# Performance work log

Hardware: AMD Instinct MI355X
Metric: run time of the kernel (lower is better)

Reference implementation:

```python
import jax, jax.numpy as jnp
import numpy as np

B, N, D, V, Y = 4, 2048, 300, 50000, 20000
MAX_REL = 10
LN_EPS = 1e-5


def setup_inputs() -> dict:
    key = jax.random.key(0)
    k1, k2, k3, k4, k5 = jax.random.split(key, 5)
    M_s = jax.random.randint(k1, (B, N), 0, V, dtype=jnp.int64)
    s = 1.0 / np.sqrt(D)
    E_v = jax.random.normal(k2, (V, D), dtype=jnp.float32) * s
    E_v = E_v.at[0].set(0.0)  # padding_idx=0
    E_y = jax.random.normal(k3, (Y, D), dtype=jnp.float32) * s
    E_y = E_y.at[0].set(0.0)
    W_A = jax.random.normal(k4, (D, D), dtype=jnp.float32) * s
    W_O = jax.random.normal(k5, (D, D), dtype=jnp.float32) * s
    gamma = jnp.ones((D,), dtype=jnp.float32)
    beta = jnp.zeros((D,), dtype=jnp.float32)
    return {"M_s": M_s, "E_v": E_v, "E_y": E_y, "W_A": W_A, "W_O": W_O,
            "gamma": gamma, "beta": beta}


def reference(M_s, E_v, E_y, W_A, W_O, gamma, beta):
    # Embedding lookup (dropout is identity in eval / p=0)
    X = E_v[M_s]                                   # [B, N, D]
    Q = X                                          # self-attention mode (v_q=None)
    # weights = Q @ W_A @ X^T
    QW = jnp.einsum('bnd,de->bne', Q, W_A)         # [B, N, D]
    weights = jnp.einsum('bne,bme->bnm', QW, X)    # [B, N, N]
    # relative-distance bias (clipped |i-j|)
    r = jnp.arange(N)
    dist = jnp.clip(jnp.abs(r[None, :] - r[:, None]), 0, MAX_REL).astype(weights.dtype)
    weights = weights - dist
    # padding mask over context (key) positions
    mask = (M_s != 0)                              # [B, N]
    weights = jnp.where(mask[:, None, :], weights, -jnp.inf)
    A = jax.nn.softmax(weights, axis=-1)           # [B, N, N]
    # contextualized query + output projection
    Q_c = jnp.einsum('bnm,bmd->bnd', A, X) @ W_O   # [B, N, D]
    # residual + layernorm over D
    H = Q_c + Q
    mu = jnp.mean(H, axis=-1, keepdims=True)
    var = jnp.mean((H - mu) ** 2, axis=-1, keepdims=True)
    Hn = (H - mu) * jax.lax.rsqrt(var + LN_EPS) * gamma + beta
    # vocab projection over senses
    y_logits = Hn @ E_y.T                          # [B, N, Y]
    return y_logits, A
```

## Files before the change

kernel.cpp:

```cpp
#include <hip/hip_runtime.h>
#include <hip/hip_bf16.h>

#define B_ 4
#define N_ 2048
#define D_ 300
#define Y_ 20000
#define ROWS (B_*N_)

typedef __attribute__((ext_vector_type(8))) short bf16x8;
typedef __attribute__((ext_vector_type(4))) float f32x4;

__device__ __forceinline__ unsigned short f2bf(float f) {
  unsigned u = __float_as_uint(f);
  unsigned r = (u + 0x7FFFu + ((u >> 16) & 1u)) >> 16;
  return (unsigned short)r;
}

__device__ __forceinline__ void gl_lds16(const unsigned short* g, unsigned short* l) {
  __builtin_amdgcn_global_load_lds(
      (const __attribute__((address_space(1))) void*)g,
      (__attribute__((address_space(3))) void*)l, 16, 0, 0);
}

__global__ __launch_bounds__(256) void k_gather_pack(const int* __restrict__ M_s,
    const float* __restrict__ E_v, float* __restrict__ X,
    unsigned short* __restrict__ Xp) {
  __shared__ float xs[320];
  int row = blockIdx.x, tid = threadIdx.x;
  int tok = M_s[row];
  const float* src = E_v + (size_t)tok * D_;
  for (int d = tid; d < 320; d += 256) xs[d] = (d < D_) ? src[d] : 0.f;
  __syncthreads();
  float* dst = X + (size_t)row * D_;
  for (int d = tid; d < D_; d += 256) dst[d] = xs[d];
  if (tid < 40) {
    int kt = tid >> 2, j = tid & 3;
    int tile = row >> 7, fb = (row >> 4) & 7, rl = row & 15;
    unsigned short v[8];
    #pragma unroll
    for (int e = 0; e < 8; ++e) v[e] = f2bf(xs[kt*32 + j*8 + e]);
    size_t off_ = ((size_t)(tile*10 + kt))*4096 + fb*512 + rl*8 + j*128;
    ushort4* o = (ushort4*)&Xp[off_];
    o[0] = make_ushort4(v[0],v[1],v[2],v[3]);
    o[1] = make_ushort4(v[4],v[5],v[6],v[7]);
  }
}

__global__ __launch_bounds__(256) void k_pack(const float* __restrict__ src,
    unsigned short* __restrict__ dst, int nrows, int ncols, int KT) {
  int chunk = blockIdx.x;
  int tile = chunk / KT, kt = chunk - tile*KT;
  size_t obase = (size_t)chunk * 4096;
  #pragma unroll
  for (int p = 0; p < 2; ++p) {
    int idx = p*256 + threadIdx.x;
    int fb = idx >> 6, l = idx & 63;
    int row = tile*128 + fb*16 + (l & 15);
    int gk = kt*32 + (l >> 4)*8;
    unsigned short v[8];
    #pragma unroll
    for (int e = 0; e < 8; ++e) {
      int k = gk + e;
      float f = (row < nrows && k < ncols) ? src[(size_t)row*ncols + k] : 0.f;
      v[e] = f2bf(f);
    }
    ushort4* o = (ushort4*)&dst[obase + (size_t)idx*8];
    o[0] = make_ushort4(v[0],v[1],v[2],v[3]);
    o[1] = make_ushort4(v[4],v[5],v[6],v[7]);
  }
}

__global__ __launch_bounds__(256) void k_packT(const float* __restrict__ src,
    unsigned short* __restrict__ dst, int src_rows, int src_cols, int KT,
    size_t src_bstride, size_t dst_bchunks) {
  __shared__ float ls[32*133];
  int chunk = blockIdx.x, b = blockIdx.y, tid = threadIdx.x;
  const float* s = src + (size_t)b * src_bstride;
  unsigned short* d = dst + ((size_t)b * dst_bchunks + chunk) * 4096;
  int tile = chunk / KT, kt = chunk - tile*KT;
  int c0 = tile*128, k0 = kt*32;
  for (int i = tid; i < 4096; i += 256) {
    int r = i >> 7, c = i & 127;
    int sr = k0 + r, sc = c0 + c;
    ls[r*133 + c] = (sr < src_rows && sc < src_cols) ? s[(size_t)sr*src_cols + sc] : 0.f;
  }
  __syncthreads();
  #pragma unroll
  for (int p = 0; p < 2; ++p) {
    int idx = p*256 + tid;
    int fb = idx >> 6, l = idx & 63;
    int r = fb*16 + (l & 15);
    int kl = (l >> 4)*8;
    unsigned short v[8];
    #pragma unroll
    for (int e = 0; e < 8; ++e) v[e] = f2bf(ls[(kl + e)*133 + r]);
    ushort4* o = (ushort4*)&d[(size_t)idx*8];
    o[0] = make_ushort4(v[0],v[1],v[2],v[3]);
    o[1] = make_ushort4(v[4],v[5],v[6],v[7]);
  }
}

template<int EPI, bool NT>
__global__ __launch_bounds__(256) void k_gemm(
    const unsigned short* __restrict__ Ap, const unsigned short* __restrict__ Bp,
    float* __restrict__ out, const float* __restrict__ resid,
    const int* __restrict__ Ms, int KT, int MTB, int NTB, int ncols)
{
  __shared__ __align__(16) union {
    unsigned short stage[2][2][4096];
    float epi[64*132];
  } sm;
  const int nt = blockIdx.x, mt = blockIdx.y, z = blockIdx.z;
  const int tid = threadIdx.x;
  const int wave = tid >> 6, lane = tid & 63;
  const int wm = wave >> 1, wn = wave & 1;
  const unsigned short* Ab = Ap + (size_t)(z*MTB + mt) * KT * 4096;
  const unsigned short* Bb = Bp + (size_t)(z*NTB + nt) * KT * 4096;
  f32x4 acc[4][4] = {};

  auto stage = [&](int s, int kt) {
    const unsigned short* ga = Ab + kt*4096 + wave*1024 + lane*8;
    const unsigned short* gb = Bb + kt*4096 + wave*1024 + lane*8;
    unsigned short* la = &sm.stage[s][0][wave*1024];
    unsigned short* lb = &sm.stage[s][1][wave*1024];
    gl_lds16(ga,       la);
    gl_lds16(ga + 512, la + 512);
    gl_lds16(gb,       lb);
    gl_lds16(gb + 512, lb + 512);
  };

  stage(0, 0);
  __syncthreads();
  for (int kt = 0; kt < KT; ++kt) {
    int cur = kt & 1;
    if (kt + 1 < KT) stage(cur ^ 1, kt + 1);
    bf16x8 af[4], bfr[4];
    #pragma unroll
    for (int i = 0; i < 4; ++i)
      af[i] = *(const bf16x8*)&sm.stage[cur][0][(wm*4 + i)*512 + lane*8];
    #pragma unroll
    for (int i = 0; i < 4; ++i)
      bfr[i] = *(const bf16x8*)&sm.stage[cur][1][(wn*4 + i)*512 + lane*8];
    #pragma unroll
    for (int mi = 0; mi < 4; ++mi)
      #pragma unroll
      for (int ni = 0; ni < 4; ++ni)
        acc[mi][ni] = __builtin_amdgcn_mfma_f32_16x16x32_bf16(
            af[mi], bfr[ni], acc[mi][ni], 0, 0, 0);
    __syncthreads();
  }

  const int lr0 = (lane >> 4) << 2;
  const int lc0 = wn*64 + (lane & 15);
  const size_t growbase = ((size_t)(z*MTB + mt)) << 7;
  #pragma unroll
  for (int h = 0; h < 2; ++h) {
    if (wm == h) {
      int tok[4];
      if (EPI == 1) {
        #pragma unroll
        for (int ni = 0; ni < 4; ++ni)
          tok[ni] = Ms[z*N_ + (nt<<7) + lc0 + ni*16];
      }
      #pragma unroll
      for (int mi = 0; mi < 4; ++mi) {
        #pragma unroll
        for (int ni = 0; ni < 4; ++ni) {
          int col = lc0 + ni*16;
          #pragma unroll
          for (int r = 0; r < 4; ++r) {
            int row = lr0 + mi*16 + r;
            float v = acc[mi][ni][r];
            if (EPI == 1) {
              int rb = (mt<<7) + h*64 + row;
              int gc = (nt<<7) + col;
              int dd = rb - gc; if (dd < 0) dd = -dd; if (dd > 10) dd = 10;
              v -= (float)dd;
              if (tok[ni] == 0) v = -3.0e38f;
            }
            sm.epi[row*132 + col] = v;
          }
        }
      }
    }
    __syncthreads();
    {
      const int r0 = tid >> 5;
      const int c4 = (tid & 31) << 2;
      const int gc = (nt << 7) + c4;
      #pragma unroll
      for (int rr = r0; rr < 64; rr += 8) {
        size_t grow = growbase + h*64 + rr;
        if (gc + 3 < ncols) {
          f32x4 v = *(const f32x4*)&sm.epi[rr*132 + c4];
          if (EPI == 2) v += *(const f32x4*)&resid[grow*(size_t)ncols + gc];
          if (NT) __builtin_nontemporal_store(v, (f32x4*)&out[grow*(size_t)ncols + gc]);
          else    *(f32x4*)&out[grow*(size_t)ncols + gc] = v;
        } else {
          #pragma unroll
          for (int e = 0; e < 4; ++e) {
            int c = gc + e;
            if (c < ncols) {
              float v = sm.epi[rr*132 + c4 + e];
              if (EPI == 2) v += resid[grow*(size_t)ncols + c];
              if (NT) __builtin_nontemporal_store(v, &out[grow*(size_t)ncols + c]);
              else    out[grow*(size_t)ncols + c] = v;
            }
          }
        }
      }
    }
    __syncthreads();
  }
}

__global__ __launch_bounds__(256) void k_softmax(float* __restrict__ S,
    unsigned short* __restrict__ Apk) {
  __shared__ float w[N_];
  __shared__ float red[4];
  int row = blockIdx.x, tid = threadIdx.x;
  float* sr = S + (size_t)row * N_;
  float vmax = -3.4e38f;
  for (int m = tid; m < N_; m += 256) { float v = sr[m]; w[m] = v; vmax = fmaxf(vmax, v); }
  #pragma unroll
  for (int off = 32; off; off >>= 1) vmax = fmaxf(vmax, __shfl_down(vmax, off, 64));
  if ((tid & 63) == 0) red[tid >> 6] = vmax;
  __syncthreads();
  vmax = fmaxf(fmaxf(red[0], red[1]), fmaxf(red[2], red[3]));
  float vsum = 0.f;
  for (int m = tid; m < N_; m += 256) {
    float e = __expf(w[m] - vmax);
    w[m] = e;
    vsum += e;
  }
  #pragma unroll
  for (int off = 32; off; off >>= 1) vsum += __shfl_down(vsum, off, 64);
  __syncthreads();
  if ((tid & 63) == 0) red[tid >> 6] = vsum;
  __syncthreads();
  float inv = 1.f / ((red[0] + red[1]) + (red[2] + red[3]));
  for (int m = tid; m < N_; m += 256)
    __builtin_nontemporal_store(w[m] * inv, &sr[m]);
  int kt = tid >> 2, j = tid & 3;
  int m0 = kt*32 + j*8;
  int fb = (row >> 4) & 7, rl = row & 15;
  unsigned short v[8];
  #pragma unroll
  for (int e = 0; e < 8; ++e) v[e] = f2bf(w[m0 + e] * inv);
  size_t off_ = ((size_t)((row >> 7)*64 + kt))*4096 + fb*512 + rl*8 + j*128;
  ushort4* o = (ushort4*)&Apk[off_];
  o[0] = make_ushort4(v[0],v[1],v[2],v[3]);
  o[1] = make_ushort4(v[4],v[5],v[6],v[7]);
}

__global__ __launch_bounds__(320) void k_ln_pack(const float* __restrict__ H,
    const float* __restrict__ gamma, const float* __restrict__ beta,
    unsigned short* __restrict__ Hp) {
  __shared__ float red[5];
  __shared__ float hs[320];
  int row = blockIdx.x, tid = threadIdx.x;
  float h = (tid < D_) ? H[(size_t)row*D_ + tid] : 0.f;
  float s = h;
  #pragma unroll
  for (int off = 32; off; off >>= 1) s += __shfl_down(s, off, 64);
  if ((tid & 63) == 0) red[tid >> 6] = s;
  __syncthreads();
  float mu = (red[0]+red[1]+red[2]+red[3]+red[4]) * (1.f/(float)D_);
  float dv = (tid < D_) ? (h - mu) : 0.f;
  float s2 = dv * dv;
  #pragma unroll
  for (int off = 32; off; off >>= 1) s2 += __shfl_down(s2, off, 64);
  __syncthreads();
  if ((tid & 63) == 0) red[tid >> 6] = s2;
  __syncthreads();
  float var = (red[0]+red[1]+red[2]+red[3]+red[4]) * (1.f/(float)D_);
  float rstd = rsqrtf(var + 1e-5f);
  hs[tid] = (tid < D_) ? (dv * rstd * gamma[tid] + beta[tid]) : 0.f;
  __syncthreads();
  if (tid < 40) {
    int kt = tid >> 2, j = tid & 3;
    int tile = row >> 7, fb = (row >> 4) & 7, rl = row & 15;
    unsigned short v[8];
    #pragma unroll
    for (int e = 0; e < 8; ++e) v[e] = f2bf(hs[kt*32 + j*8 + e]);
    size_t off_ = ((size_t)(tile*10 + kt))*4096 + fb*512 + rl*8 + j*128;
    ushort4* o = (ushort4*)&Hp[off_];
    o[0] = make_ushort4(v[0],v[1],v[2],v[3]);
    o[1] = make_ushort4(v[4],v[5],v[6],v[7]);
  }
}

extern "C" void kernel_launch(void* const* d_in, const int* in_sizes, int n_in,
                              void* d_out, int out_size, void* d_ws, size_t ws_size,
                              hipStream_t stream) {
  const int*   M_s   = (const int*)d_in[0];
  const float* E_v   = (const float*)d_in[1];
  const float* E_y   = (const float*)d_in[2];
  const float* W_A   = (const float*)d_in[3];
  const float* W_O   = (const float*)d_in[4];
  const float* gamma = (const float*)d_in[5];
  const float* beta  = (const float*)d_in[6];

  float* Yl = (float*)d_out;
  float* A  = Yl + (size_t)ROWS * Y_;

  float* X  = (float*)d_ws;
  float* QW = X  + (size_t)ROWS * D_;
  float* C  = QW;
  float* H  = QW + (size_t)ROWS * D_;
  unsigned short* Ep = (unsigned short*)(H + (size_t)ROWS * D_);
  unsigned short* Hpk = (unsigned short*)X;

  unsigned short* scr = (unsigned short*)(Yl + 100000000ull);
  unsigned short* Xp  = scr;
  unsigned short* QWp = Xp  + 2621440;
  unsigned short* Wap = QWp + 2621440;
  unsigned short* Wop = Wap + 122880;
  unsigned short* XTp = Wop + 122880;
  unsigned short* Cp  = XTp + 3145728;
  unsigned short* Apk = Cp  + 2621440;

  k_gather_pack<<<ROWS, 256, 0, stream>>>(M_s, E_v, X, Xp);
  k_packT <<<dim3(3*10,1), 256, 0, stream>>>(W_A, Wap, D_, D_, 10, 0, 0);
  k_gemm<0,false><<<dim3(3,64,1), 256, 0, stream>>>(Xp, Wap, QW, nullptr, nullptr, 10, 64, 3, D_);
  k_pack  <<<64*10, 256, 0, stream>>>(QW, QWp, ROWS, D_, 10);
  k_gemm<1,false><<<dim3(16,16,4), 256, 0, stream>>>(QWp, Xp, A, nullptr, M_s, 10, 16, 16, N_);
  k_softmax<<<ROWS, 256, 0, stream>>>(A, Apk);
  k_packT <<<dim3(3*64,4), 256, 0, stream>>>(X, XTp, N_, D_, 64, (size_t)N_*D_, 192);
  k_gemm<0,false><<<dim3(3,16,4), 256, 0, stream>>>(Apk, XTp, C, nullptr, nullptr, 64, 16, 3, D_);
  k_pack  <<<64*10, 256, 0, stream>>>(C, Cp, ROWS, D_, 10);
  k_packT <<<dim3(3*10,1), 256, 0, stream>>>(W_O, Wop, D_, D_, 10, 0, 0);
  k_gemm<2,false><<<dim3(3,64,1), 256, 0, stream>>>(Cp, Wop, H, X, nullptr, 10, 64, 3, D_);
  k_ln_pack<<<ROWS, 320, 0, stream>>>(H, gamma, beta, Hpk);
  k_pack  <<<157*10, 256, 0, stream>>>(E_y, Ep, Y_, D_, 10);
  k_gemm<0,true><<<dim3(157,64,1), 256, 0, stream>>>(Hpk, Ep, Yl, nullptr, nullptr, 10, 64, 157, Y_);
}
```

Before: 436.0 us.

## Fuse bf16 packing into GEMM epilogues, load A via registers, swizzle vocab GEMM grid

The QW and context GEMMs now write their outputs directly in the packed bf16 tile layout, so the two separate pack kernels and their fp32 round trips through memory go away. The GEMM main loop now loads A fragments straight from global memory into registers, stages only B through LDS, and is unrolled by two for double buffering. The large vocab-projection GEMM uses a 1D grid with a blockIdx swizzle that groups column tiles to improve L2 reuse. Risks include extra register pressure and A loads no longer going through LDS, though each wave reads only its own A rows anyway.

```diff
diff --git a/kernel.cpp b/kernel.cpp
--- a/kernel.cpp
+++ b/kernel.cpp
@@ -100,54 +100,70 @@
   }
 }
 
-template<int EPI, bool NT>
+template<int EPI, bool NT, bool PACKOUT, bool SWZ>
 __global__ __launch_bounds__(256) void k_gemm(
     const unsigned short* __restrict__ Ap, const unsigned short* __restrict__ Bp,
-    float* __restrict__ out, const float* __restrict__ resid,
-    const int* __restrict__ Ms, int KT, int MTB, int NTB, int ncols)
+    float* __restrict__ out, unsigned short* __restrict__ outp,
+    const float* __restrict__ resid, const int* __restrict__ Ms,
+    int KT, int KTd, int MTB, int NTB, int ncols)
 {
   __shared__ __align__(16) union {
-    unsigned short stage[2][2][4096];
+    unsigned short stage[2][4096];
     float epi[64*132];
   } sm;
-  const int nt = blockIdx.x, mt = blockIdx.y, z = blockIdx.z;
+  int nt, mt, z;
+  if (SWZ) {
+    int nwg = MTB * NTB;
+    int wg = blockIdx.x;
+    int cpx = nwg >> 3;
+    int swz = (wg & 7) * cpx + (wg >> 3);
+    mt = swz % MTB; nt = swz / MTB; z = 0;
+  } else {
+    nt = blockIdx.x; mt = blockIdx.y; z = blockIdx.z;
+  }
   const int tid = threadIdx.x;
   const int wave = tid >> 6, lane = tid & 63;
   const int wm = wave >> 1, wn = wave & 1;
   const unsigned short* Ab = Ap + (size_t)(z*MTB + mt) * KT * 4096;
   const unsigned short* Bb = Bp + (size_t)(z*NTB + nt) * KT * 4096;
   f32x4 acc[4][4] = {};
-
-  auto stage = [&](int s, int kt) {
-    const unsigned short* ga = Ab + kt*4096 + wave*1024 + lane*8;
+  bf16x8 aA[4], aB[4];
+
+  auto stageB = [&](int s, int kt) {
     const unsigned short* gb = Bb + kt*4096 + wave*1024 + lane*8;
-    unsigned short* la = &sm.stage[s][0][wave*1024];
-    unsigned short* lb = &sm.stage[s][1][wave*1024];
-    gl_lds16(ga,       la);
-    gl_lds16(ga + 512, la + 512);
+    unsigned short* lb = &sm.stage[s][wave*1024];
     gl_lds16(gb,       lb);
     gl_lds16(gb + 512, lb + 512);
   };
-
-  stage(0, 0);
-  __syncthreads();
-  for (int kt = 0; kt < KT; ++kt) {
-    int cur = kt & 1;
-    if (kt + 1 < KT) stage(cur ^ 1, kt + 1);
-    bf16x8 af[4], bfr[4];
+  auto loadA = [&](int kt, bf16x8* d) {
+    const unsigned short* ga = Ab + kt*4096 + (wm*4)*512 + lane*8;
+    #pragma unroll
+    for (int i = 0; i < 4; ++i) d[i] = *(const bf16x8*)(ga + i*512);
+  };
+  auto mfma_step = [&](int cur, const bf16x8* a) {
+    bf16x8 bfr[4];
     #pragma unroll
     for (int i = 0; i < 4; ++i)
-      af[i] = *(const bf16x8*)&sm.stage[cur][0][(wm*4 + i)*512 + lane*8];
-    #pragma unroll
-    for (int i = 0; i < 4; ++i)
-      bfr[i] = *(const bf16x8*)&sm.stage[cur][1][(wn*4 + i)*512 + lane*8];
+      bfr[i] = *(const bf16x8*)&sm.stage[cur][(wn*4 + i)*512 + lane*8];
     #pragma unroll
     for (int mi = 0; mi < 4; ++mi)
       #pragma unroll
       for (int ni = 0; ni < 4; ++ni)
         acc[mi][ni] = __builtin_amdgcn_mfma_f32_16x16x32_bf16(
-            af[mi], bfr[ni], acc[mi][ni], 0, 0, 0);
+            a[mi], bfr[ni], acc[mi][ni], 0, 0, 0);
+  };
+
+  stageB(0, 0); loadA(0, aA);
+  __syncthreads();
+  for (int kt = 0; kt < KT; kt += 2) {
+    if (kt + 1 < KT) { stageB(1, kt + 1); loadA(kt + 1, aB); }
+    mfma_step(0, aA);
     __syncthreads();
+    if (kt + 1 < KT) {
+      if (kt + 2 < KT) { stageB(0, kt + 2); loadA(kt + 2, aA); }
+      mfma_step(1, aB);
+      __syncthreads();
+    }
   }
 
   const int lr0 = (lane >> 4) << 2;
@@ -184,7 +200,25 @@
       }
     }
     __syncthreads();
-    {
+    if (PACKOUT) {
+      int prow = tid >> 2, pktq = tid & 3;
+      int ktd = nt*4 + pktq;
+      if (ktd < KTd) {
+        int grl = h*64 + prow;
+        int fb = grl >> 4, rl = grl & 15;
+        size_t cbase = ((size_t)((z*MTB + mt)*KTd + ktd))*4096 + fb*512 + rl*8;
+        #pragma unroll
+        for (int oct = 0; oct < 4; ++oct) {
+          unsigned short v[8];
+          #pragma unroll
+          for (int e = 0; e < 8; ++e)
+            v[e] = f2bf(sm.epi[prow*132 + pktq*32 + oct*8 + e]);
+          ushort4* o = (ushort4*)&outp[cbase + oct*128];
+          o[0] = make_ushort4(v[0],v[1],v[2],v[3]);
+          o[1] = make_ushort4(v[4],v[5],v[6],v[7]);
+        }
+      }
+    } else {
       const int r0 = tid >> 5;
       const int c4 = (tid & 31) << 2;
       const int gc = (nt << 7) + c4;
@@ -306,7 +340,6 @@
 
   float* X  = (float*)d_ws;
   float* QW = X  + (size_t)ROWS * D_;
-  float* C  = QW;
   float* H  = QW + (size_t)ROWS * D_;
   unsigned short* Ep = (unsigned short*)(H + (size_t)ROWS * D_);
   unsigned short* Hpk = (unsigned short*)X;
@@ -322,16 +355,19 @@
 
   k_gather_pack<<<ROWS, 256, 0, stream>>>(M_s, E_v, X, Xp);
   k_packT <<<dim3(3*10,1), 256, 0, stream>>>(W_A, Wap, D_, D_, 10, 0, 0);
-  k_gemm<0,false><<<dim3(3,64,1), 256, 0, stream>>>(Xp, Wap, QW, nullptr, nullptr, 10, 64, 3, D_);
-  k_pack  <<<64*10, 256, 0, stream>>>(QW, QWp, ROWS, D_, 10);
-  k_gemm<1,false><<<dim3(16,16,4), 256, 0, stream>>>(QWp, Xp, A, nullptr, M_s, 10, 16, 16, N_);
+  k_gemm<0,false,true,false><<<dim3(3,64,1), 256, 0, stream>>>(
+      Xp, Wap, nullptr, QWp, nullptr, nullptr, 10, 10, 64, 3, D_);
+  k_gemm<1,false,false,false><<<dim3(16,16,4), 256, 0, stream>>>(
+      QWp, Xp, A, nullptr, nullptr, M_s, 10, 0, 16, 16, N_);
   k_softmax<<<ROWS, 256, 0, stream>>>(A, Apk);
   k_packT <<<dim3(3*64,4), 256, 0, stream>>>(X, XTp, N_, D_, 64, (size_t)N_*D_, 192);
-  k_gemm<0,false><<<dim3(3,16,4), 256, 0, stream>>>(Apk, XTp, C, nullptr, nullptr, 64, 16, 3, D_);
-  k_pack  <<<64*10, 256, 0, stream>>>(C, Cp, ROWS, D_, 10);
+  k_gemm<0,false,true,false><<<dim3(3,16,4), 256, 0, stream>>>(
+      Apk, XTp, nullptr, Cp, nullptr, nullptr, 64, 10, 16, 3, D_);
   k_packT <<<dim3(3*10,1), 256, 0, stream>>>(W_O, Wop, D_, D_, 10, 0, 0);
-  k_gemm<2,false><<<dim3(3,64,1), 256, 0, stream>>>(Cp, Wop, H, X, nullptr, 10, 64, 3, D_);
+  k_gemm<2,false,false,false><<<dim3(3,64,1), 256, 0, stream>>>(
+      Cp, Wop, H, nullptr, X, nullptr, 10, 0, 64, 3, D_);
   k_ln_pack<<<ROWS, 320, 0, stream>>>(H, gamma, beta, Hpk);
   k_pack  <<<157*10, 256, 0, stream>>>(E_y, Ep, Y_, D_, 10);
-  k_gemm<0,true><<<dim3(157,64,1), 256, 0, stream>>>(Hpk, Ep, Yl, nullptr, nullptr, 10, 64, 157, Y_);
-}
+  k_gemm<0,true,false,true><<<dim3(157*64,1,1), 256, 0, stream>>>(
+      Hpk, Ep, Yl, nullptr, nullptr, nullptr, 10, 0, 64, 157, Y_);
+}
```

Result: slower. 455.0 us (+4.3%).
